# Performance work log

Measured on AMD Instinct MI355X. Metric: run time of the kernel, lower is better.

Reference implementation:

```python
import jax, jax.numpy as jnp
import numpy as np

N = 4_000_000
F = 8   # EXPERIMENTS['full'] feature count
H = 16  # hidden width of both MLPs
NBINS = 28


def _lin_init(k, i, o):
    return jax.random.normal(k, (i, o), jnp.float32) * (1.0 / np.sqrt(i))


def setup_inputs() -> dict:
    key = jax.random.key(0)
    ks = jax.random.split(key, 16)
    inp = {
        "x_feat": jax.random.normal(ks[0], (N, F), jnp.float32),
        # mh MLP params
        "mh_W1": _lin_init(ks[1], F, H), "mh_b1": jnp.zeros((H,), jnp.float32),
        "mh_W2": _lin_init(ks[2], H, H), "mh_b2": jnp.zeros((H,), jnp.float32),
        "mh_W3": _lin_init(ks[3], H, 1), "mh_b3": jnp.zeros((1,), jnp.float32),
        # mh_less MLP params (input dim 1 = Size)
        "ml_W1": _lin_init(ks[4], 1, H), "ml_b1": jnp.zeros((H,), jnp.float32),
        "ml_W2": _lin_init(ks[5], H, H), "ml_b2": jnp.zeros((H,), jnp.float32),
        "ml_W3": _lin_init(ks[6], H, 1), "ml_b3": jnp.zeros((1,), jnp.float32),
    }
    # deletion sizes in 1..40 (some > 28 exercise the skip branch)
    del_lens = jax.random.randint(ks[7], (N,), 1, 41, jnp.int32)
    eq = jax.random.bernoulli(ks[8], 0.3, (N,))
    alt = jax.random.randint(ks[9], (N,), 1, 41, jnp.int32)
    inp["del_lens"] = del_lens
    inp["mh_len"] = jnp.where(eq, del_lens, alt).astype(jnp.int32)
    return inp


def _mlp(x, W1, b1, W2, b2, W3, b3):
    h = jax.nn.sigmoid(x @ W1 + b1)
    h = jax.nn.sigmoid(h @ W2 + b2)
    return h @ W3 + b3  # [N, 1]


def reference(x_feat, mh_W1, mh_b1, mh_W2, mh_b2, mh_W3, mh_b3,
              ml_W1, ml_b1, ml_W2, ml_b2, ml_W3, ml_b3,
              del_lens, mh_len):
    dl_f = del_lens.astype(x_feat.dtype)[:, None]  # [N,1]
    # psi score: exp(phi - dl*0.25)
    mh_scores = jnp.exp(_mlp(x_feat, mh_W1, mh_b1, mh_W2, mh_b2, mh_W3, mh_b3)
                        - dl_f * 0.25)[:, 0]  # [N]
    # mh_less score on Size, added only where del_len == homologyLength
    mhless = jnp.exp(_mlp(dl_f, ml_W1, ml_b1, ml_W2, ml_b2, ml_W3, ml_b3)
                     - dl_f * 0.25)[:, 0]  # [N]
    mhfull_contribution = jnp.where(del_lens == mh_len, mhless, 0.0)
    y_mh_phi = mh_scores + mhfull_contribution  # [N]

    # mh_less scores for dl = 1..28
    dls = jnp.arange(1, NBINS + 1, dtype=x_feat.dtype)[:, None]  # [28,1]
    dl2_scores = jnp.exp(_mlp(dls, ml_W1, ml_b1, ml_W2, ml_b2, ml_W3, ml_b3)
                         - dls * 0.25)[:, 0]  # [28]

    # scatter-add mh_scores into bin (dl-1), skipping dl > 28
    vals = jnp.where(del_lens <= NBINS, mh_scores, 0.0)
    seg = jnp.clip(del_lens - 1, 0, NBINS - 1)
    mh_contribution = jax.ops.segment_sum(vals, seg, num_segments=NBINS)
    y_mh_less_phi = dl2_scores + mh_contribution  # [28]

    return (y_mh_phi, y_mh_less_phi)
```

## Files before the change

### kernel.cpp

```cpp
#include <hip/hip_runtime.h>
#include <math.h>

#define NBINS 28
#define L2E 1.44269504088896340736f

#define EXP2F(x) __builtin_amdgcn_exp2f(x)
#define RCPF(x)  __builtin_amdgcn_rcpf(x)
#define SCHED_FENCE() __builtin_amdgcn_sched_barrier(0)

#define WS_TBL 0
#define WS_W1  64
#define WS_B1  192
#define WS_W2  208
#define WS_B2  464
#define WS_W3  480
#define WS_B3  496
#define WS_TOT 512

__global__ void prep_kernel(const float* __restrict__ mh_W1, const float* __restrict__ mh_b1,
                            const float* __restrict__ mh_W2, const float* __restrict__ mh_b2,
                            const float* __restrict__ mh_W3, const float* __restrict__ mh_b3,
                            const float* __restrict__ ml_W1, const float* __restrict__ ml_b1,
                            const float* __restrict__ ml_W2, const float* __restrict__ ml_b2,
                            const float* __restrict__ ml_W3, const float* __restrict__ ml_b3,
                            float* __restrict__ ws, float* __restrict__ out_bins) {
    const int t = threadIdx.x;
    for (int k = t; k < 128; k += 64) ws[WS_W1 + k] = -L2E * mh_W1[k];
    for (int k = t; k < 16;  k += 64) ws[WS_B1 + k] = -L2E * mh_b1[k];
    for (int k = t; k < 256; k += 64) ws[WS_W2 + k] = -L2E * mh_W2[k];
    for (int k = t; k < 16;  k += 64) ws[WS_B2 + k] = -L2E * mh_b2[k];
    for (int k = t; k < 16;  k += 64) ws[WS_W3 + k] =  L2E * mh_W3[k];
    if (t == 0) ws[WS_B3] = L2E * mh_b3[0];

    if (t < 40) {
        const float x = (float)(t + 1);
        float h1[16], h2[16];
        #pragma unroll
        for (int j = 0; j < 16; ++j)
            h1[j] = 1.0f / (1.0f + expf(-(x * ml_W1[j] + ml_b1[j])));
        #pragma unroll
        for (int j = 0; j < 16; ++j) {
            float a = ml_b2[j];
            #pragma unroll
            for (int k = 0; k < 16; ++k) a = fmaf(h1[k], ml_W2[k * 16 + j], a);
            h2[j] = 1.0f / (1.0f + expf(-a));
        }
        float phi = ml_b3[0];
        #pragma unroll
        for (int k = 0; k < 16; ++k) phi = fmaf(h2[k], ml_W3[k], phi);
        const float sc = expf(phi - 0.25f * x);
        ws[WS_TBL + t] = sc;
        if (t < NBINS) out_bins[t] = sc;
    }
}

__global__ __launch_bounds__(256) void main_kernel(
        const float4* __restrict__ x4,
        const int2* __restrict__ dl2p,
        const int2* __restrict__ ml2p,
        const float* __restrict__ ws,
        float2* __restrict__ out2,
        float* __restrict__ out_bins,
        int npair) {
    __shared__ float s_tbl[40];
    __shared__ float s_bins[4 * NBINS];
    const int tid = threadIdx.x;
    if (tid < 40) s_tbl[tid] = ws[WS_TBL + tid];
    if (tid < 4 * NBINS) s_bins[tid] = 0.0f;
    __syncthreads();

    const int p = blockIdx.x * 256 + tid;
    const bool active = (p < npair);
    const int pc = active ? p : 0;

    const float4 a0 = x4[4 * pc + 0];
    const float4 a1 = x4[4 * pc + 1];
    const float4 b0 = x4[4 * pc + 2];
    const float4 b1 = x4[4 * pc + 3];
    const int2 dl = dl2p[pc];
    const int2 ml = ml2p[pc];
    const float xf0[8] = {a0.x, a0.y, a0.z, a0.w, a1.x, a1.y, a1.z, a1.w};
    const float xf1[8] = {b0.x, b0.y, b0.z, b0.w, b1.x, b1.y, b1.z, b1.w};

    float u0[16], u1[16];
    #pragma unroll
    for (int j = 0; j < 16; ++j) {
        const float b = ws[WS_B1 + j];
        u0[j] = b; u1[j] = b;
    }
    SCHED_FENCE();
    #pragma unroll
    for (int f = 0; f < 8; ++f) {
        #pragma unroll
        for (int j = 0; j < 16; ++j) {
            const float w = ws[WS_W1 + f * 16 + j];
            u0[j] = fmaf(xf0[f], w, u0[j]);
            u1[j] = fmaf(xf1[f], w, u1[j]);
        }
        if (f & 1) SCHED_FENCE();
    }
    float h0[16], h1[16];
    #pragma unroll
    for (int j = 0; j < 16; ++j) {
        h0[j] = RCPF(1.0f + EXP2F(u0[j]));
        h1[j] = RCPF(1.0f + EXP2F(u1[j]));
    }

    float v0[16], v1[16];
    #pragma unroll
    for (int j = 0; j < 16; ++j) {
        const float b = ws[WS_B2 + j];
        v0[j] = b; v1[j] = b;
    }
    SCHED_FENCE();
    #pragma unroll
    for (int k = 0; k < 16; ++k) {
        #pragma unroll
        for (int j = 0; j < 16; ++j) {
            const float w = ws[WS_W2 + k * 16 + j];
            v0[j] = fmaf(h0[k], w, v0[j]);
            v1[j] = fmaf(h1[k], w, v1[j]);
        }
        if (k & 1) SCHED_FENCE();
    }

    float phi0 = ws[WS_B3], phi1 = phi0;
    #pragma unroll
    for (int j = 0; j < 16; ++j) {
        const float w3 = ws[WS_W3 + j];
        phi0 = fmaf(RCPF(1.0f + EXP2F(v0[j])), w3, phi0);
        phi1 = fmaf(RCPF(1.0f + EXP2F(v1[j])), w3, phi1);
    }
    const float sc0 = EXP2F(fmaf((float)dl.x, -0.25f * L2E, phi0));
    const float sc1 = EXP2F(fmaf((float)dl.y, -0.25f * L2E, phi1));

    if (active) {
        const int i0 = min(max(dl.x, 1), 40) - 1;
        const int i1 = min(max(dl.y, 1), 40) - 1;
        const float add0 = (dl.x == ml.x) ? s_tbl[i0] : 0.0f;
        const float add1 = (dl.y == ml.y) ? s_tbl[i1] : 0.0f;
        out2[p] = make_float2(sc0 + add0, sc1 + add1);
        float* myb = &s_bins[(tid >> 6) * NBINS];
        if (dl.x >= 1 && dl.x <= NBINS) unsafeAtomicAdd(&myb[dl.x - 1], sc0);
        if (dl.y >= 1 && dl.y <= NBINS) unsafeAtomicAdd(&myb[dl.y - 1], sc1);
    }

    __syncthreads();
    if (tid < NBINS) {
        const float bsum = s_bins[tid] + s_bins[NBINS + tid] +
                           s_bins[2 * NBINS + tid] + s_bins[3 * NBINS + tid];
        unsafeAtomicAdd(&out_bins[tid], bsum);
    }
}

extern "C" void kernel_launch(void* const* d_in, const int* in_sizes, int n_in,
                              void* d_out, int out_size, void* d_ws, size_t ws_size,
                              hipStream_t stream) {
    const int n = in_sizes[0] / 8;

    const float* x_feat = (const float*)d_in[0];
    const float* mh_W1  = (const float*)d_in[1];
    const float* mh_b1  = (const float*)d_in[2];
    const float* mh_W2  = (const float*)d_in[3];
    const float* mh_b2  = (const float*)d_in[4];
    const float* mh_W3  = (const float*)d_in[5];
    const float* mh_b3  = (const float*)d_in[6];
    const float* ml_W1  = (const float*)d_in[7];
    const float* ml_b1  = (const float*)d_in[8];
    const float* ml_W2  = (const float*)d_in[9];
    const float* ml_b2  = (const float*)d_in[10];
    const float* ml_W3  = (const float*)d_in[11];
    const float* ml_b3  = (const float*)d_in[12];
    const int* del_lens = (const int*)d_in[13];
    const int* mh_len   = (const int*)d_in[14];

    float* out      = (float*)d_out;
    float* out_bins = out + n;
    float* ws       = (float*)d_ws;

    prep_kernel<<<dim3(1), dim3(64), 0, stream>>>(
        mh_W1, mh_b1, mh_W2, mh_b2, mh_W3, mh_b3,
        ml_W1, ml_b1, ml_W2, ml_b2, ml_W3, ml_b3,
        ws, out_bins);

    const int npair = n / 2;
    const int nblocks = (npair + 255) / 256;
    main_kernel<<<dim3(nblocks), dim3(256), 0, stream>>>(
        (const float4*)x_feat, (const int2*)del_lens, (const int2*)mh_len,
        ws, (float2*)out, out_bins, npair);
}
```

Baseline: 310.7 us.

## Process four rows per thread using packed FP32 FMA for MLP layers

Each thread now handles four rows instead of two. The two dense layers use packed two-wide FMA (v_pk_fma_f32) on row pairs, so one instruction covers two rows and the per-row FMA instruction count is halved. Loads and stores widen to int4/float4, and the grid shrinks by half. The cost is higher register pressure and fewer waves in flight, which may hurt latency hiding. The exp and rcp sigmoid work stays scalar.

```diff
diff --git a/kernel.cpp b/kernel.cpp
--- a/kernel.cpp
+++ b/kernel.cpp
@@ -7,6 +7,14 @@
 #define EXP2F(x) __builtin_amdgcn_exp2f(x)
 #define RCPF(x)  __builtin_amdgcn_rcpf(x)
 #define SCHED_FENCE() __builtin_amdgcn_sched_barrier(0)
+
+typedef float v2f __attribute__((ext_vector_type(2)));
+
+static __device__ __forceinline__ v2f splat2(float w) { v2f r; r.x = w; r.y = w; return r; }
+static __device__ __forceinline__ v2f make2(float a, float b) { v2f r; r.x = a; r.y = b; return r; }
+static __device__ __forceinline__ v2f pkfma(v2f a, v2f b, v2f c) {
+    return __builtin_elementwise_fma(a, b, c);
+}
 
 #define WS_TBL 0
 #define WS_W1  64
@@ -56,12 +64,12 @@
 
 __global__ __launch_bounds__(256) void main_kernel(
         const float4* __restrict__ x4,
-        const int2* __restrict__ dl2p,
-        const int2* __restrict__ ml2p,
+        const int4* __restrict__ dl4p,
+        const int4* __restrict__ ml4p,
         const float* __restrict__ ws,
-        float2* __restrict__ out2,
+        float4* __restrict__ out4,
         float* __restrict__ out_bins,
-        int npair) {
+        int nquad) {
     __shared__ float s_tbl[40];
     __shared__ float s_bins[4 * NBINS];
     const int tid = threadIdx.x;
@@ -69,48 +77,53 @@
     if (tid < 4 * NBINS) s_bins[tid] = 0.0f;
     __syncthreads();
 
-    const int p = blockIdx.x * 256 + tid;
-    const bool active = (p < npair);
-    const int pc = active ? p : 0;
-
-    const float4 a0 = x4[4 * pc + 0];
-    const float4 a1 = x4[4 * pc + 1];
-    const float4 b0 = x4[4 * pc + 2];
-    const float4 b1 = x4[4 * pc + 3];
-    const int2 dl = dl2p[pc];
-    const int2 ml = ml2p[pc];
-    const float xf0[8] = {a0.x, a0.y, a0.z, a0.w, a1.x, a1.y, a1.z, a1.w};
-    const float xf1[8] = {b0.x, b0.y, b0.z, b0.w, b1.x, b1.y, b1.z, b1.w};
-
-    float u0[16], u1[16];
+    const int q = blockIdx.x * 256 + tid;
+    const bool active = (q < nquad);
+    const int qc = active ? q : 0;
+
+    float xf[4][8];
+    #pragma unroll
+    for (int r = 0; r < 4; ++r) {
+        const float4 a = x4[8 * qc + 2 * r + 0];
+        const float4 b = x4[8 * qc + 2 * r + 1];
+        xf[r][0] = a.x; xf[r][1] = a.y; xf[r][2] = a.z; xf[r][3] = a.w;
+        xf[r][4] = b.x; xf[r][5] = b.y; xf[r][6] = b.z; xf[r][7] = b.w;
+    }
+    const int4 dl = dl4p[qc];
+    const int4 ml = ml4p[qc];
+
+    v2f u01[16], u23[16];
     #pragma unroll
     for (int j = 0; j < 16; ++j) {
         const float b = ws[WS_B1 + j];
-        u0[j] = b; u1[j] = b;
+        u01[j] = splat2(b); u23[j] = splat2(b);
     }
     SCHED_FENCE();
     #pragma unroll
     for (int f = 0; f < 8; ++f) {
+        const v2f x01 = make2(xf[0][f], xf[1][f]);
+        const v2f x23 = make2(xf[2][f], xf[3][f]);
         #pragma unroll
         for (int j = 0; j < 16; ++j) {
             const float w = ws[WS_W1 + f * 16 + j];
-            u0[j] = fmaf(xf0[f], w, u0[j]);
-            u1[j] = fmaf(xf1[f], w, u1[j]);
+            const v2f ww = splat2(w);
+            u01[j] = pkfma(x01, ww, u01[j]);
+            u23[j] = pkfma(x23, ww, u23[j]);
         }
         if (f & 1) SCHED_FENCE();
     }
-    float h0[16], h1[16];
-    #pragma unroll
-    for (int j = 0; j < 16; ++j) {
-        h0[j] = RCPF(1.0f + EXP2F(u0[j]));
-        h1[j] = RCPF(1.0f + EXP2F(u1[j]));
-    }
-
-    float v0[16], v1[16];
+    v2f h01[16], h23[16];
+    #pragma unroll
+    for (int j = 0; j < 16; ++j) {
+        h01[j] = make2(RCPF(1.0f + EXP2F(u01[j].x)), RCPF(1.0f + EXP2F(u01[j].y)));
+        h23[j] = make2(RCPF(1.0f + EXP2F(u23[j].x)), RCPF(1.0f + EXP2F(u23[j].y)));
+    }
+
+    v2f v01[16], v23[16];
     #pragma unroll
     for (int j = 0; j < 16; ++j) {
         const float b = ws[WS_B2 + j];
-        v0[j] = b; v1[j] = b;
+        v01[j] = splat2(b); v23[j] = splat2(b);
     }
     SCHED_FENCE();
     #pragma unroll
@@ -118,31 +131,45 @@
         #pragma unroll
         for (int j = 0; j < 16; ++j) {
             const float w = ws[WS_W2 + k * 16 + j];
-            v0[j] = fmaf(h0[k], w, v0[j]);
-            v1[j] = fmaf(h1[k], w, v1[j]);
+            const v2f ww = splat2(w);
+            v01[j] = pkfma(h01[k], ww, v01[j]);
+            v23[j] = pkfma(h23[k], ww, v23[j]);
         }
         if (k & 1) SCHED_FENCE();
     }
 
-    float phi0 = ws[WS_B3], phi1 = phi0;
+    const float pb = ws[WS_B3];
+    v2f phi01 = splat2(pb), phi23 = splat2(pb);
     #pragma unroll
     for (int j = 0; j < 16; ++j) {
         const float w3 = ws[WS_W3 + j];
-        phi0 = fmaf(RCPF(1.0f + EXP2F(v0[j])), w3, phi0);
-        phi1 = fmaf(RCPF(1.0f + EXP2F(v1[j])), w3, phi1);
-    }
-    const float sc0 = EXP2F(fmaf((float)dl.x, -0.25f * L2E, phi0));
-    const float sc1 = EXP2F(fmaf((float)dl.y, -0.25f * L2E, phi1));
+        const v2f ww = splat2(w3);
+        const v2f s01 = make2(RCPF(1.0f + EXP2F(v01[j].x)), RCPF(1.0f + EXP2F(v01[j].y)));
+        const v2f s23 = make2(RCPF(1.0f + EXP2F(v23[j].x)), RCPF(1.0f + EXP2F(v23[j].y)));
+        phi01 = pkfma(s01, ww, phi01);
+        phi23 = pkfma(s23, ww, phi23);
+    }
+    const float sc0 = EXP2F(fmaf((float)dl.x, -0.25f * L2E, phi01.x));
+    const float sc1 = EXP2F(fmaf((float)dl.y, -0.25f * L2E, phi01.y));
+    const float sc2 = EXP2F(fmaf((float)dl.z, -0.25f * L2E, phi23.x));
+    const float sc3 = EXP2F(fmaf((float)dl.w, -0.25f * L2E, phi23.y));
 
     if (active) {
         const int i0 = min(max(dl.x, 1), 40) - 1;
         const int i1 = min(max(dl.y, 1), 40) - 1;
-        const float add0 = (dl.x == ml.x) ? s_tbl[i0] : 0.0f;
-        const float add1 = (dl.y == ml.y) ? s_tbl[i1] : 0.0f;
-        out2[p] = make_float2(sc0 + add0, sc1 + add1);
+        const int i2 = min(max(dl.z, 1), 40) - 1;
+        const int i3 = min(max(dl.w, 1), 40) - 1;
+        float4 o;
+        o.x = sc0 + ((dl.x == ml.x) ? s_tbl[i0] : 0.0f);
+        o.y = sc1 + ((dl.y == ml.y) ? s_tbl[i1] : 0.0f);
+        o.z = sc2 + ((dl.z == ml.z) ? s_tbl[i2] : 0.0f);
+        o.w = sc3 + ((dl.w == ml.w) ? s_tbl[i3] : 0.0f);
+        out4[q] = o;
         float* myb = &s_bins[(tid >> 6) * NBINS];
         if (dl.x >= 1 && dl.x <= NBINS) unsafeAtomicAdd(&myb[dl.x - 1], sc0);
         if (dl.y >= 1 && dl.y <= NBINS) unsafeAtomicAdd(&myb[dl.y - 1], sc1);
+        if (dl.z >= 1 && dl.z <= NBINS) unsafeAtomicAdd(&myb[dl.z - 1], sc2);
+        if (dl.w >= 1 && dl.w <= NBINS) unsafeAtomicAdd(&myb[dl.w - 1], sc3);
     }
 
     __syncthreads();
@@ -183,9 +210,9 @@
         ml_W1, ml_b1, ml_W2, ml_b2, ml_W3, ml_b3,
         ws, out_bins);
 
-    const int npair = n / 2;
-    const int nblocks = (npair + 255) / 256;
+    const int nquad = n / 4;
+    const int nblocks = (nquad + 255) / 256;
     main_kernel<<<dim3(nblocks), dim3(256), 0, stream>>>(
-        (const float4*)x_feat, (const int2*)del_lens, (const int2*)mh_len,
-        ws, (float2*)out, out_bins, npair);
-}
+        (const float4*)x_feat, (const int4*)del_lens, (const int4*)mh_len,
+        ws, (float4*)out, out_bins, nquad);
+}
```

Result: no change. 315.6 us (+1.6%).

## Use packed fp16 dot2 for the MLP hidden layers

Applied to the files above, without the earlier changes.

Prepacks layer-1 and layer-2 weights as fp16 pairs in the workspace and converts inputs and hidden activations to packed fp16, then uses v_dot2 (fp16x2 multiply with fp32 accumulate) in place of scalar FMAs. This halves the FMA instruction count for the two matrix layers and the number of weight scalar loads. The scheduling fences are removed. The cost is reduced precision on inputs, weights and activations, which may exceed the tolerance, plus extra pack and convert instructions.

```diff
diff --git a/kernel.cpp b/kernel.cpp
--- a/kernel.cpp
+++ b/kernel.cpp
@@ -6,7 +6,18 @@
 
 #define EXP2F(x) __builtin_amdgcn_exp2f(x)
 #define RCPF(x)  __builtin_amdgcn_rcpf(x)
-#define SCHED_FENCE() __builtin_amdgcn_sched_barrier(0)
+
+typedef __fp16 h2t __attribute__((ext_vector_type(2)));
+
+static __device__ __forceinline__ float fdot2(h2t a, h2t b, float c) {
+    return __builtin_amdgcn_fdot2(a, b, c, false);
+}
+static __device__ __forceinline__ h2t pkx(float lo, float hi) {
+    return __builtin_amdgcn_cvt_pkrtz(lo, hi);
+}
+static __device__ __forceinline__ h2t asH2(float f) {
+    union { float f; h2t h; } u; u.f = f; return u.h;
+}
 
 #define WS_TBL 0
 #define WS_W1  64
@@ -15,7 +26,9 @@
 #define WS_B2  464
 #define WS_W3  480
 #define WS_B3  496
-#define WS_TOT 512
+#define WP_W1  512
+#define WP_W2  576
+#define WS_TOT 704
 
 __global__ void prep_kernel(const float* __restrict__ mh_W1, const float* __restrict__ mh_b1,
                             const float* __restrict__ mh_W2, const float* __restrict__ mh_b2,
@@ -32,6 +45,21 @@
     for (int k = t; k < 16;  k += 64) ws[WS_W3 + k] =  L2E * mh_W3[k];
     if (t == 0) ws[WS_B3] = L2E * mh_b3[0];
 
+    for (int k = t; k < 64; k += 64) {
+        const int f2 = k >> 4, j = k & 15;
+        union { __fp16 h[2]; float f; } u;
+        u.h[0] = (__fp16)(-L2E * mh_W1[(2 * f2)     * 16 + j]);
+        u.h[1] = (__fp16)(-L2E * mh_W1[(2 * f2 + 1) * 16 + j]);
+        ws[WP_W1 + k] = u.f;
+    }
+    for (int k = t; k < 128; k += 64) {
+        const int k2 = k >> 4, j = k & 15;
+        union { __fp16 h[2]; float f; } u;
+        u.h[0] = (__fp16)(-L2E * mh_W2[(2 * k2)     * 16 + j]);
+        u.h[1] = (__fp16)(-L2E * mh_W2[(2 * k2 + 1) * 16 + j]);
+        ws[WP_W2 + k] = u.f;
+    }
+
     if (t < 40) {
         const float x = (float)(t + 1);
         float h1[16], h2[16];
@@ -79,8 +107,12 @@
     const float4 b1 = x4[4 * pc + 3];
     const int2 dl = dl2p[pc];
     const int2 ml = ml2p[pc];
-    const float xf0[8] = {a0.x, a0.y, a0.z, a0.w, a1.x, a1.y, a1.z, a1.w};
-    const float xf1[8] = {b0.x, b0.y, b0.z, b0.w, b1.x, b1.y, b1.z, b1.w};
+
+    h2t xp0[4], xp1[4];
+    xp0[0] = pkx(a0.x, a0.y); xp0[1] = pkx(a0.z, a0.w);
+    xp0[2] = pkx(a1.x, a1.y); xp0[3] = pkx(a1.z, a1.w);
+    xp1[0] = pkx(b0.x, b0.y); xp1[1] = pkx(b0.z, b0.w);
+    xp1[2] = pkx(b1.x, b1.y); xp1[3] = pkx(b1.z, b1.w);
 
     float u0[16], u1[16];
     #pragma unroll
@@ -88,22 +120,24 @@
         const float b = ws[WS_B1 + j];
         u0[j] = b; u1[j] = b;
     }
-    SCHED_FENCE();
-    #pragma unroll
-    for (int f = 0; f < 8; ++f) {
+    #pragma unroll
+    for (int f2 = 0; f2 < 4; ++f2) {
         #pragma unroll
         for (int j = 0; j < 16; ++j) {
-            const float w = ws[WS_W1 + f * 16 + j];
-            u0[j] = fmaf(xf0[f], w, u0[j]);
-            u1[j] = fmaf(xf1[f], w, u1[j]);
+            const h2t w = asH2(ws[WP_W1 + f2 * 16 + j]);
+            u0[j] = fdot2(xp0[f2], w, u0[j]);
+            u1[j] = fdot2(xp1[f2], w, u1[j]);
         }
-        if (f & 1) SCHED_FENCE();
-    }
-    float h0[16], h1[16];
-    #pragma unroll
-    for (int j = 0; j < 16; ++j) {
-        h0[j] = RCPF(1.0f + EXP2F(u0[j]));
-        h1[j] = RCPF(1.0f + EXP2F(u1[j]));
+    }
+    h2t hp0[8], hp1[8];
+    #pragma unroll
+    for (int k2 = 0; k2 < 8; ++k2) {
+        const float h0a = RCPF(1.0f + EXP2F(u0[2 * k2]));
+        const float h0b = RCPF(1.0f + EXP2F(u0[2 * k2 + 1]));
+        const float h1a = RCPF(1.0f + EXP2F(u1[2 * k2]));
+        const float h1b = RCPF(1.0f + EXP2F(u1[2 * k2 + 1]));
+        hp0[k2] = pkx(h0a, h0b);
+        hp1[k2] = pkx(h1a, h1b);
     }
 
     float v0[16], v1[16];
@@ -112,16 +146,14 @@
         const float b = ws[WS_B2 + j];
         v0[j] = b; v1[j] = b;
     }
-    SCHED_FENCE();
-    #pragma unroll
-    for (int k = 0; k < 16; ++k) {
+    #pragma unroll
+    for (int k2 = 0; k2 < 8; ++k2) {
         #pragma unroll
         for (int j = 0; j < 16; ++j) {
-            const float w = ws[WS_W2 + k * 16 + j];
-            v0[j] = fmaf(h0[k], w, v0[j]);
-            v1[j] = fmaf(h1[k], w, v1[j]);
+            const h2t w = asH2(ws[WP_W2 + k2 * 16 + j]);
+            v0[j] = fdot2(hp0[k2], w, v0[j]);
+            v1[j] = fdot2(hp1[k2], w, v1[j]);
         }
-        if (k & 1) SCHED_FENCE();
     }
 
     float phi0 = ws[WS_B3], phi1 = phi0;
```

After: 311.6 us. Within noise of the previous version (+0.3%).
